# Optimization experiments

Measured on AMD Instinct MI355X. Metric: run time of the kernel, lower is better.

The kernel has to match this reference:

```python
import jax, jax.numpy as jnp
import numpy as np

N_ = 50000   # nodes
E_ = 800000  # edges
G_ = 64      # graphs in batch
EPS = 1e-5   # batchnorm eps


def _lin(k, fi, fo):
    s = 1.0 / np.sqrt(fi)
    return jax.random.uniform(k, (fi, fo), jnp.float32, -s, s)


def setup_inputs() -> dict:
    key = jax.random.key(0)
    ks = jax.random.split(key, 16)
    d_in, d_h, d_out = 128, 128, 5000
    inp = {
        'x': jax.random.normal(ks[0], (N_, d_in), jnp.float32),
        'edge_index': jax.random.randint(ks[1], (2, E_), 0, N_, jnp.int32),
        'batch': jnp.sort(jax.random.randint(ks[2], (N_,), 0, G_, jnp.int32)),
    }
    dims = [(d_in, d_h), (d_h, d_h), (d_h, d_h), (d_h, d_h)]
    for i, (fi, fo) in enumerate(dims, 1):
        inp[f'w{i}'] = _lin(ks[2 + i], fi, fo)
        inp[f'b{i}'] = jnp.zeros((fo,), jnp.float32)
        inp[f'g{i}'] = jnp.ones((fo,), jnp.float32)   # BN gamma
        inp[f'be{i}'] = jnp.zeros((fo,), jnp.float32)  # BN beta
    inp['gw1'] = _lin(ks[7], d_h, d_h // 2)
    inp['gb1'] = jnp.zeros((d_h // 2,), jnp.float32)
    inp['gw2'] = _lin(ks[8], d_h // 2, 1)
    inp['gb2'] = jnp.zeros((1,), jnp.float32)
    inp['cw'] = _lin(ks[9], d_h, d_out)
    inp['cb'] = jnp.zeros((d_out,), jnp.float32)
    return inp


def reference(x, w1, b1, g1, be1, w2, b2, g2, be2, w3, b3, g3, be3,
              w4, b4, g4, be4, gw1, gb1, gw2, gb2, cw, cb,
              edge_index, batch):
    # GCN normalization with self-loops (PyG GCNConv semantics)
    loops = jnp.arange(N_, dtype=edge_index.dtype)
    src = jnp.concatenate([edge_index[0], loops])
    dst = jnp.concatenate([edge_index[1], loops])
    deg = jax.ops.segment_sum(jnp.ones(src.shape[0], jnp.float32), dst, N_)
    dis = jax.lax.rsqrt(jnp.maximum(deg, 1.0))  # deg >= 1 with self-loops
    norm = dis[src] * dis[dst]                  # [E+N]

    def gcn(h, w, b):
        hw = h @ w                              # [N, d]
        msg = hw[src] * norm[:, None]           # gather over edges
        return jax.ops.segment_sum(msg, dst, N_) + b

    def bn(h, g, be):
        m = h.mean(0)
        v = h.var(0)                            # biased var (training BN)
        return (h - m) * jax.lax.rsqrt(v + EPS) * g + be

    h = x
    for w, b, g, be in ((w1, b1, g1, be1), (w2, b2, g2, be2),
                        (w3, b3, g3, be3), (w4, b4, g4, be4)):
        h = jax.nn.relu(bn(gcn(h, w, b), g, be))  # dropout is identity (eval)

    # attention pooling: per-graph softmax over gate scores
    gate = jax.nn.relu(h @ gw1 + gb1) @ gw2 + gb2  # [N, 1]
    gate = gate[:, 0]
    m = jax.ops.segment_max(gate, batch, G_)
    e = jnp.exp(gate - m[batch])
    s = jax.ops.segment_sum(e, batch, G_)
    a = e / s[batch]                               # [N]
    pooled = jax.ops.segment_sum(h * a[:, None], batch, G_)  # [G, d]
    return pooled @ cw + cb                        # [G, out]
```

## Files before the change

kernel.cpp:

```cpp
#include <hip/hip_runtime.h>
#include <hip/hip_bf16.h>
#include <hip/hip_fp16.h>

#define NN   50000
#define NE   800000
#define NG   64
#define DH   128
#define DOUT 5000
#define BNEPS 1e-5f
#define NBLK 196
#define KB   32

__global__ __launch_bounds__(256) void k_count(const int* __restrict__ dst, int* __restrict__ cnt) {
    int e = blockIdx.x * 256 + threadIdx.x;
    if (e < NE) atomicAdd(&cnt[dst[e]], 1);
}

__global__ __launch_bounds__(256) void k_blkscan(const int* __restrict__ cnt, int* __restrict__ rowptr,
                                                 int* __restrict__ bsum) {
    __shared__ int s[256];
    int t = threadIdx.x, i = blockIdx.x * 256 + t;
    int v = (i < NN) ? cnt[i] : 0;
    s[t] = v;
    __syncthreads();
    for (int off = 1; off < 256; off <<= 1) {
        int x = (t >= off) ? s[t - off] : 0;
        __syncthreads();
        s[t] += x;
        __syncthreads();
    }
    if (i < NN) rowptr[i] = s[t] - v;
    if (t == 255) bsum[blockIdx.x] = s[255];
}

__global__ __launch_bounds__(256) void k_bscan(const int* __restrict__ bsum, int* __restrict__ boff) {
    __shared__ int s[256];
    int t = threadIdx.x;
    int v = (t < NBLK) ? bsum[t] : 0;
    s[t] = v;
    __syncthreads();
    for (int off = 1; off < 256; off <<= 1) {
        int x = (t >= off) ? s[t - off] : 0;
        __syncthreads();
        s[t] += x;
        __syncthreads();
    }
    if (t < NBLK) boff[t] = s[t] - v;
}

__global__ __launch_bounds__(256) void k_fin(int* __restrict__ rowptr, const int* __restrict__ boff,
                                             int* __restrict__ cnt, float* __restrict__ dis) {
    int i = blockIdx.x * 256 + threadIdx.x;
    if (i >= NN) { if (i == NN) rowptr[NN] = NE; return; }
    rowptr[i] += boff[blockIdx.x];
    dis[i] = rsqrtf((float)(cnt[i] + 1));
    cnt[i] = 0;
}

__global__ __launch_bounds__(256) void k_fill(const int* __restrict__ ei, const int* __restrict__ rowptr,
                                              int* __restrict__ fil, const float* __restrict__ dis,
                                              int* __restrict__ col, float* __restrict__ wgt) {
    int e = blockIdx.x * 256 + threadIdx.x;
    if (e >= NE) return;
    int s = ei[e], d = ei[NE + e];
    int p = rowptr[d] + atomicAdd(&fil[d], 1);
    col[p] = s;
    wgt[p] = dis[s] * dis[d];
}

__global__ __launch_bounds__(256) void k_gemm2(const float* __restrict__ X, const float* __restrict__ W,
                                               const float* __restrict__ scale, const float* __restrict__ shift,
                                               __half* __restrict__ Y) {
    __shared__ float Xt[KB][DH + 1];
    __shared__ float Ws[KB][DH];
    int t = threadIdx.x;
    int row0 = blockIdx.x * 128;
    int ra = (t >> 4) * 4;
    int ca = (t & 15) * 4;
    float acc[8][8];
#pragma unroll
    for (int i = 0; i < 8; i++)
#pragma unroll
        for (int j = 0; j < 8; j++) acc[i][j] = 0.f;

    for (int kt = 0; kt < DH / KB; kt++) {
        __syncthreads();
#pragma unroll
        for (int i = 0; i < 4; i++) {
            int f = t + i * 256;
            int row = f >> 3;
            int kq = f & 7;
            int grow = min(row0 + row, NN - 1);
            float4 v = ((const float4*)X)[grow * (DH / 4) + kt * 8 + kq];
            if (scale) {
                float4 sc = ((const float4*)scale)[kt * 8 + kq];
                float4 sh = ((const float4*)shift)[kt * 8 + kq];
                v.x = fmaxf(fmaf(v.x, sc.x, sh.x), 0.f);
                v.y = fmaxf(fmaf(v.y, sc.y, sh.y), 0.f);
                v.z = fmaxf(fmaf(v.z, sc.z, sh.z), 0.f);
                v.w = fmaxf(fmaf(v.w, sc.w, sh.w), 0.f);
            }
            Xt[kq * 4 + 0][row] = v.x;
            Xt[kq * 4 + 1][row] = v.y;
            Xt[kq * 4 + 2][row] = v.z;
            Xt[kq * 4 + 3][row] = v.w;
        }
#pragma unroll
        for (int i = 0; i < 4; i++) {
            int f = t + i * 256;
            int k = f >> 5;
            int cq = f & 31;
            float4 wv = ((const float4*)W)[(kt * KB + k) * (DH / 4) + cq];
            *(float4*)&Ws[k][cq * 4] = wv;
        }
        __syncthreads();
#pragma unroll 8
        for (int k = 0; k < KB; k++) {
            float ar[8], bc[8];
            ar[0] = Xt[k][ra + 0];  ar[1] = Xt[k][ra + 1];
            ar[2] = Xt[k][ra + 2];  ar[3] = Xt[k][ra + 3];
            ar[4] = Xt[k][ra + 64]; ar[5] = Xt[k][ra + 65];
            ar[6] = Xt[k][ra + 66]; ar[7] = Xt[k][ra + 67];
            float4 b0 = *(const float4*)&Ws[k][ca];
            float4 b1 = *(const float4*)&Ws[k][ca + 64];
            bc[0] = b0.x; bc[1] = b0.y; bc[2] = b0.z; bc[3] = b0.w;
            bc[4] = b1.x; bc[5] = b1.y; bc[6] = b1.z; bc[7] = b1.w;
#pragma unroll
            for (int ri = 0; ri < 8; ri++)
#pragma unroll
                for (int ci = 0; ci < 8; ci++)
                    acc[ri][ci] = fmaf(ar[ri], bc[ci], acc[ri][ci]);
        }
    }
#pragma unroll
    for (int ri = 0; ri < 8; ri++) {
        int row = row0 + ((ri < 4) ? (ra + ri) : (ra + 60 + ri));
        if (row < NN) {
            __half hv[8];
#pragma unroll
            for (int ci = 0; ci < 8; ci++) hv[ci] = __float2half(acc[ri][ci]);
            *(int2*)(Y + row * DH + ca) = *(int2*)hv;
            *(int2*)(Y + row * DH + ca + 64) = *(int2*)(hv + 4);
        }
    }
}

__global__ __launch_bounds__(256) void k_agg(const __half* __restrict__ HW, const int* __restrict__ rowptr,
                                             const int* __restrict__ col, const float* __restrict__ wgt,
                                             const float* __restrict__ dis, const float* __restrict__ bias,
                                             float* __restrict__ OUT, float* __restrict__ ssum,
                                             float* __restrict__ ssq) {
    __shared__ float lsum[DH], lsq[DH];
    int t = threadIdx.x;
    if (t < DH) { lsum[t] = 0.f; lsq[t] = 0.f; }
    __syncthreads();
    int wid = t >> 6, lane = t & 63;
    int sub = lane >> 5, sl = lane & 31;
    const int2* HW4 = (const int2*)HW;
    float4* OUT4 = (float4*)OUT;
    float4 bv = ((const float4*)bias)[sl];
    float s0 = 0, s1 = 0, s2 = 0, s3 = 0, q0 = 0, q1 = 0, q2 = 0, q3 = 0;
    int gw = blockIdx.x * 4 + wid;
    for (int i = gw * 2 + sub; i < NN; i += 16384) {
        float sd = dis[i];
        int2 hr = HW4[i * 32 + sl];
        float2 f0 = __half22float2(*(__half2*)&hr.x);
        float2 f1 = __half22float2(*(__half2*)&hr.y);
        float a0 = sd * sd * f0.x, a1 = sd * sd * f0.y;
        float a2 = sd * sd * f1.x, a3 = sd * sd * f1.y;
        int p = rowptr[i], p1 = rowptr[i + 1];
        for (; p + 4 <= p1; p += 4) {
            int c0 = col[p], c1 = col[p + 1], c2 = col[p + 2], c3 = col[p + 3];
            float w0 = wgt[p], w1 = wgt[p + 1], w2 = wgt[p + 2], w3 = wgt[p + 3];
            int2 r0 = HW4[c0 * 32 + sl];
            int2 r1 = HW4[c1 * 32 + sl];
            int2 r2 = HW4[c2 * 32 + sl];
            int2 r3 = HW4[c3 * 32 + sl];
            float2 g0 = __half22float2(*(__half2*)&r0.x), g1 = __half22float2(*(__half2*)&r0.y);
            a0 = fmaf(w0, g0.x, a0); a1 = fmaf(w0, g0.y, a1); a2 = fmaf(w0, g1.x, a2); a3 = fmaf(w0, g1.y, a3);
            g0 = __half22float2(*(__half2*)&r1.x); g1 = __half22float2(*(__half2*)&r1.y);
            a0 = fmaf(w1, g0.x, a0); a1 = fmaf(w1, g0.y, a1); a2 = fmaf(w1, g1.x, a2); a3 = fmaf(w1, g1.y, a3);
            g0 = __half22float2(*(__half2*)&r2.x); g1 = __half22float2(*(__half2*)&r2.y);
            a0 = fmaf(w2, g0.x, a0); a1 = fmaf(w2, g0.y, a1); a2 = fmaf(w2, g1.x, a2); a3 = fmaf(w2, g1.y, a3);
            g0 = __half22float2(*(__half2*)&r3.x); g1 = __half22float2(*(__half2*)&r3.y);
            a0 = fmaf(w3, g0.x, a0); a1 = fmaf(w3, g0.y, a1); a2 = fmaf(w3, g1.x, a2); a3 = fmaf(w3, g1.y, a3);
        }
        for (; p < p1; p++) {
            int c = col[p];
            float wv = wgt[p];
            int2 r = HW4[c * 32 + sl];
            float2 g0 = __half22float2(*(__half2*)&r.x), g1 = __half22float2(*(__half2*)&r.y);
            a0 = fmaf(wv, g0.x, a0); a1 = fmaf(wv, g0.y, a1);
            a2 = fmaf(wv, g1.x, a2); a3 = fmaf(wv, g1.y, a3);
        }
        a0 += bv.x; a1 += bv.y; a2 += bv.z; a3 += bv.w;
        OUT4[i * 32 + sl] = make_float4(a0, a1, a2, a3);
        s0 += a0; s1 += a1; s2 += a2; s3 += a3;
        q0 += a0 * a0; q1 += a1 * a1; q2 += a2 * a2; q3 += a3 * a3;
    }
    atomicAdd(&lsum[sl * 4 + 0], s0); atomicAdd(&lsum[sl * 4 + 1], s1);
    atomicAdd(&lsum[sl * 4 + 2], s2); atomicAdd(&lsum[sl * 4 + 3], s3);
    atomicAdd(&lsq[sl * 4 + 0], q0);  atomicAdd(&lsq[sl * 4 + 1], q1);
    atomicAdd(&lsq[sl * 4 + 2], q2);  atomicAdd(&lsq[sl * 4 + 3], q3);
    __syncthreads();
    if (t < DH) { atomicAdd(&ssum[t], lsum[t]); atomicAdd(&ssq[t], lsq[t]); }
}

__global__ void k_bnfin(const float* __restrict__ ssum, const float* __restrict__ ssq,
                        const float* __restrict__ g, const float* __restrict__ be,
                        float* __restrict__ scale, float* __restrict__ shift) {
    int f = threadIdx.x;
    float m = ssum[f] * (1.f / NN);
    float v = ssq[f] * (1.f / NN) - m * m;
    float r = rsqrtf(v + BNEPS);
    float sc = r * g[f];
    scale[f] = sc;
    shift[f] = fmaf(-m, sc, be[f]);
}

__global__ __launch_bounds__(256) void k_bnrelu(float* __restrict__ A, const float* __restrict__ scale,
                                                const float* __restrict__ shift) {
    __shared__ float sc[DH], sh[DH];
    if (threadIdx.x < DH) { sc[threadIdx.x] = scale[threadIdx.x]; sh[threadIdx.x] = shift[threadIdx.x]; }
    __syncthreads();
    float4* A4 = (float4*)A;
    const int total = NN * (DH / 4);
    for (int i = blockIdx.x * 256 + threadIdx.x; i < total; i += gridDim.x * 256) {
        int f = (i & 31) * 4;
        float4 v = A4[i];
        v.x = fmaxf(fmaf(v.x, sc[f], sh[f]), 0.f);
        v.y = fmaxf(fmaf(v.y, sc[f + 1], sh[f + 1]), 0.f);
        v.z = fmaxf(fmaf(v.z, sc[f + 2], sh[f + 2]), 0.f);
        v.w = fmaxf(fmaf(v.w, sc[f + 3], sh[f + 3]), 0.f);
        A4[i] = v;
    }
}

__global__ __launch_bounds__(256) void k_gate(const float* __restrict__ H, const float* __restrict__ gw1,
                                              const float* __restrict__ gb1, const float* __restrict__ gw2,
                                              const float* __restrict__ gb2, float* __restrict__ gate) {
    __shared__ float w1s[DH * 64];
    __shared__ float rowbuf[4][DH];
    int t = threadIdx.x;
    for (int i = t; i < DH * 64; i += 256) w1s[i] = gw1[i];
    __syncthreads();
    int wid = t >> 6, lane = t & 63;
    float b1v = gb1[lane], w2v = gw2[lane], b2v = gb2[0];
    int nw = gridDim.x * 4;
    int iters = (NN + nw - 1) / nw;
    const float2* H2 = (const float2*)H;
    for (int it = 0; it < iters; it++) {
        int i = blockIdx.x * 4 + wid + it * nw;
        bool act = i < NN;
        if (act) {
            float2 hv = H2[i * 64 + lane];
            rowbuf[wid][lane * 2] = hv.x;
            rowbuf[wid][lane * 2 + 1] = hv.y;
        }
        __syncthreads();
        float hid = 0.f;
#pragma unroll 8
        for (int k = 0; k < DH; k++) hid = fmaf(rowbuf[wid][k], w1s[k * 64 + lane], hid);
        hid = fmaxf(hid + b1v, 0.f);
        float v = hid * w2v;
        for (int off = 32; off > 0; off >>= 1) v += __shfl_down(v, off, 64);
        if (act && lane == 0) gate[i] = v + b2v;
        __syncthreads();
    }
}

__device__ __forceinline__ int lbound(const int* __restrict__ a, int v) {
    int lo = 0, hi = NN;
    while (lo < hi) {
        int mid = (lo + hi) >> 1;
        if (a[mid] < v) lo = mid + 1; else hi = mid;
    }
    return lo;
}

__global__ __launch_bounds__(256) void k_pms(const float* __restrict__ gate, const int* __restrict__ batch,
                                             float* __restrict__ ms) {
    __shared__ float red[256];
    int g = blockIdx.x, t = threadIdx.x;
    int s = lbound(batch, g), e = lbound(batch, g + 1);
    float m = -INFINITY;
    for (int i = s + t; i < e; i += 256) m = fmaxf(m, gate[i]);
    red[t] = m; __syncthreads();
    for (int off = 128; off > 0; off >>= 1) { if (t < off) red[t] = fmaxf(red[t], red[t + off]); __syncthreads(); }
    m = red[0];
    __syncthreads();
    float se = 0.f;
    for (int i = s + t; i < e; i += 256) se += __expf(gate[i] - m);
    red[t] = se; __syncthreads();
    for (int off = 128; off > 0; off >>= 1) { if (t < off) red[t] += red[t + off]; __syncthreads(); }
    if (t == 0) {
        ms[g * 2] = m;
        ms[g * 2 + 1] = (e > s) ? 1.f / red[0] : 0.f;
    }
}

#define PNODES 8
__global__ __launch_bounds__(256) void k_pool2(const float* __restrict__ H, const float* __restrict__ gate,
                                               const int* __restrict__ batch, const float* __restrict__ ms,
                                               float* __restrict__ pooled) {
    int wid = threadIdx.x >> 6, lane = threadIdx.x & 63;
    int base = (blockIdx.x * 4 + wid) * PNODES;
    if (base >= NN) return;
    int end = min(base + PNODES, NN);
    const float2* H2 = (const float2*)H;
    float2 acc = make_float2(0.f, 0.f);
    int curg = batch[base];
    for (int i = base; i < end; i++) {
        int g = batch[i];
        if (g != curg) {
            atomicAdd(&pooled[curg * DH + lane * 2], acc.x);
            atomicAdd(&pooled[curg * DH + lane * 2 + 1], acc.y);
            acc = make_float2(0.f, 0.f);
            curg = g;
        }
        float a = __expf(gate[i] - ms[g * 2]) * ms[g * 2 + 1];
        float2 h = H2[i * 64 + lane];
        acc.x = fmaf(a, h.x, acc.x);
        acc.y = fmaf(a, h.y, acc.y);
    }
    atomicAdd(&pooled[curg * DH + lane * 2], acc.x);
    atomicAdd(&pooled[curg * DH + lane * 2 + 1], acc.y);
}

__global__ __launch_bounds__(256) void k_cls(const float* __restrict__ pooled, const float* __restrict__ cw,
                                             const float* __restrict__ cb, float* __restrict__ out) {
    __shared__ float pr[DH];
    int g = blockIdx.y;
    if (threadIdx.x < DH) pr[threadIdx.x] = pooled[g * DH + threadIdx.x];
    __syncthreads();
    int j = blockIdx.x * 256 + threadIdx.x;
    if (j >= DOUT) return;
    float acc = cb[j];
#pragma unroll 8
    for (int k = 0; k < DH; k++) acc = fmaf(pr[k], cw[k * DOUT + j], acc);
    out[g * DOUT + j] = acc;
}

extern "C" void kernel_launch(void* const* d_in, const int* in_sizes, int n_in,
                              void* d_out, int out_size, void* d_ws, size_t ws_size,
                              hipStream_t stream) {
    const float* x     = (const float*)d_in[0];
    const int*   ei    = (const int*)d_in[1];
    const int*   batch = (const int*)d_in[2];
    const float* w[4]  = {(const float*)d_in[3], (const float*)d_in[7], (const float*)d_in[11], (const float*)d_in[15]};
    const float* bb[4] = {(const float*)d_in[4], (const float*)d_in[8], (const float*)d_in[12], (const float*)d_in[16]};
    const float* gg[4] = {(const float*)d_in[5], (const float*)d_in[9], (const float*)d_in[13], (const float*)d_in[17]};
    const float* be[4] = {(const float*)d_in[6], (const float*)d_in[10], (const float*)d_in[14], (const float*)d_in[18]};
    const float* gw1 = (const float*)d_in[19];
    const float* gb1 = (const float*)d_in[20];
    const float* gw2 = (const float*)d_in[21];
    const float* gb2 = (const float*)d_in[22];
    const float* cw  = (const float*)d_in[23];
    const float* cb  = (const float*)d_in[24];

    char* base = (char*)d_ws;
    size_t off = 0;
    auto take = [&](size_t n) -> char* { char* r = base + off; off = (off + n + 255) & ~(size_t)255; return r; };
    float*  bufA   = (float*)take((size_t)NN * DH * 4);
    __half* bufB   = (__half*)take((size_t)NN * DH * 2);
    int*   colv   = (int*)take((size_t)NE * 4);
    float* wgt    = (float*)take((size_t)NE * 4);
    int*   rowptr = (int*)take((size_t)(NN + 1) * 4);
    int*   cnt    = (int*)take((size_t)NN * 4);
    float* dis    = (float*)take((size_t)NN * 4);
    float* gate   = (float*)take((size_t)NN * 4);
    float* stats  = (float*)take(2 * DH * 4);
    float* ssum = stats, *ssq = stats + DH;
    float* scale  = (float*)take(DH * 4);
    float* shift  = (float*)take(DH * 4);
    float* pooled = (float*)take((size_t)NG * DH * 4);
    int*   bsum   = (int*)take((size_t)256 * 4);
    int*   boff   = (int*)take((size_t)256 * 4);
    float* ms     = (float*)take((size_t)NG * 2 * 4);

    hipMemsetAsync(cnt, 0, NN * 4, stream);
    k_count<<<(NE + 255) / 256, 256, 0, stream>>>(ei + NE, cnt);
    k_blkscan<<<NBLK, 256, 0, stream>>>(cnt, rowptr, bsum);
    k_bscan<<<1, 256, 0, stream>>>(bsum, boff);
    k_fin<<<NBLK, 256, 0, stream>>>(rowptr, boff, cnt, dis);
    k_fill<<<(NE + 255) / 256, 256, 0, stream>>>(ei, rowptr, cnt, dis, colv, wgt);

    const int gemm_grid = (NN + 127) / 128;
    for (int L = 0; L < 4; L++) {
        k_gemm2<<<gemm_grid, 256, 0, stream>>>(L == 0 ? x : bufA, w[L],
                                               L == 0 ? nullptr : scale,
                                               L == 0 ? nullptr : shift, bufB);
        hipMemsetAsync(stats, 0, 2 * DH * 4, stream);
        k_agg<<<2048, 256, 0, stream>>>(bufB, rowptr, colv, wgt, dis, bb[L], bufA, ssum, ssq);
        k_bnfin<<<1, DH, 0, stream>>>(ssum, ssq, gg[L], be[L], scale, shift);
    }
    k_bnrelu<<<2048, 256, 0, stream>>>(bufA, scale, shift);
    k_gate<<<1024, 256, 0, stream>>>(bufA, gw1, gb1, gw2, gb2, gate);
    k_pms<<<NG, 256, 0, stream>>>(gate, batch, ms);
    hipMemsetAsync(pooled, 0, (size_t)NG * DH * 4, stream);
    k_pool2<<<(NN + 4 * PNODES - 1) / (4 * PNODES), 256, 0, stream>>>(bufA, gate, batch, ms, pooled);
    k_cls<<<dim3((DOUT + 255) / 256, NG), 256, 0, stream>>>(pooled, cw, cb, (float*)d_out);
}
```

Measured before the change: 658.6 us.

## Use fp16 MFMA for layer GEMMs and fold final BN-ReLU into consumers

Replaces the FP32 register-tiled SIMT GEMM with an MFMA 16x16x32 f16 kernel. The weights are pre-transposed to fp16 once per call, and each lane loads its A and B fragments straight from global memory with no shared-memory staging. The standalone final BN+ReLU pass is removed: the gate and pooling kernels now apply scale and shift on the fly. Stats and pooled zeroing move into bnfin and pms, which drops per-layer memset launches. Converting the inputs to fp16 lowers precision, and fragments fetched uncoalesced from global memory may strain bandwidth.

New measurement: 604.9 us. -8.2%, faster.

```diff
diff --git a/kernel.cpp b/kernel.cpp
--- a/kernel.cpp
+++ b/kernel.cpp
@@ -9,7 +9,9 @@
 #define DOUT 5000
 #define BNEPS 1e-5f
 #define NBLK 196
-#define KB   32
+
+typedef _Float16 h8 __attribute__((ext_vector_type(8)));
+typedef float    f4 __attribute__((ext_vector_type(4)));
 
 __global__ __launch_bounds__(256) void k_count(const int* __restrict__ dst, int* __restrict__ cnt) {
     int e = blockIdx.x * 256 + threadIdx.x;
@@ -68,79 +70,82 @@
     wgt[p] = dis[s] * dis[d];
 }
 
-__global__ __launch_bounds__(256) void k_gemm2(const float* __restrict__ X, const float* __restrict__ W,
+__global__ __launch_bounds__(256) void k_wprep(const float* __restrict__ W0, const float* __restrict__ W1,
+                                               const float* __restrict__ W2, const float* __restrict__ W3,
+                                               __half* __restrict__ Wt) {
+    const float* Ws[4] = {W0, W1, W2, W3};
+    int m = blockIdx.x >> 4;
+    int chunk = blockIdx.x & 15;
+    const float* W = Ws[m];
+    __half* O = Wt + m * DH * DH;
+    int o = chunk * 1024 + threadIdx.x;
+    for (int r = 0; r < 4; r++, o += 256) {
+        int c = o >> 7, k = o & 127;
+        O[o] = __float2half(W[k * DH + c]);
+    }
+}
+
+__global__ __launch_bounds__(256) void k_gemm3(const float* __restrict__ X, const __half* __restrict__ Wt,
                                                const float* __restrict__ scale, const float* __restrict__ shift,
                                                __half* __restrict__ Y) {
-    __shared__ float Xt[KB][DH + 1];
-    __shared__ float Ws[KB][DH];
     int t = threadIdx.x;
-    int row0 = blockIdx.x * 128;
-    int ra = (t >> 4) * 4;
-    int ca = (t & 15) * 4;
-    float acc[8][8];
-#pragma unroll
-    for (int i = 0; i < 8; i++)
-#pragma unroll
-        for (int j = 0; j < 8; j++) acc[i][j] = 0.f;
-
-    for (int kt = 0; kt < DH / KB; kt++) {
-        __syncthreads();
-#pragma unroll
-        for (int i = 0; i < 4; i++) {
-            int f = t + i * 256;
-            int row = f >> 3;
-            int kq = f & 7;
-            int grow = min(row0 + row, NN - 1);
-            float4 v = ((const float4*)X)[grow * (DH / 4) + kt * 8 + kq];
+    int lane = t & 63, wid = t >> 6;
+    int wr = wid >> 1, wc = wid & 1;
+    int row0 = blockIdx.x * 64;
+    int lr = lane & 15, lk = (lane >> 4) * 8;
+
+    f4 acc[2][4];
+#pragma unroll
+    for (int i = 0; i < 2; i++)
+#pragma unroll
+        for (int j = 0; j < 4; j++) acc[i][j] = (f4){0.f, 0.f, 0.f, 0.f};
+
+    for (int kt = 0; kt < 4; kt++) {
+        int kbase = kt * 32 + lk;
+        h8 afr[2];
+#pragma unroll
+        for (int fr = 0; fr < 2; fr++) {
+            int gr = row0 + wr * 32 + fr * 16 + lr;
+            gr = min(gr, NN - 1);
+            const float4* p = (const float4*)(X + (size_t)gr * DH + kbase);
+            float4 v0 = p[0], v1 = p[1];
             if (scale) {
-                float4 sc = ((const float4*)scale)[kt * 8 + kq];
-                float4 sh = ((const float4*)shift)[kt * 8 + kq];
-                v.x = fmaxf(fmaf(v.x, sc.x, sh.x), 0.f);
-                v.y = fmaxf(fmaf(v.y, sc.y, sh.y), 0.f);
-                v.z = fmaxf(fmaf(v.z, sc.z, sh.z), 0.f);
-                v.w = fmaxf(fmaf(v.w, sc.w, sh.w), 0.f);
+                const float4* sc4 = (const float4*)(scale + kbase);
+                const float4* sh4 = (const float4*)(shift + kbase);
+                float4 s0 = sc4[0], s1 = sc4[1], h0 = sh4[0], h1 = sh4[1];
+                v0.x = fmaxf(fmaf(v0.x, s0.x, h0.x), 0.f);
+                v0.y = fmaxf(fmaf(v0.y, s0.y, h0.y), 0.f);
+                v0.z = fmaxf(fmaf(v0.z, s0.z, h0.z), 0.f);
+                v0.w = fmaxf(fmaf(v0.w, s0.w, h0.w), 0.f);
+                v1.x = fmaxf(fmaf(v1.x, s1.x, h1.x), 0.f);
+                v1.y = fmaxf(fmaf(v1.y, s1.y, h1.y), 0.f);
+                v1.z = fmaxf(fmaf(v1.z, s1.z, h1.z), 0.f);
+                v1.w = fmaxf(fmaf(v1.w, s1.w, h1.w), 0.f);
             }
-            Xt[kq * 4 + 0][row] = v.x;
-            Xt[kq * 4 + 1][row] = v.y;
-            Xt[kq * 4 + 2][row] = v.z;
-            Xt[kq * 4 + 3][row] = v.w;
-        }
-#pragma unroll
-        for (int i = 0; i < 4; i++) {
-            int f = t + i * 256;
-            int k = f >> 5;
-            int cq = f & 31;
-            float4 wv = ((const float4*)W)[(kt * KB + k) * (DH / 4) + cq];
-            *(float4*)&Ws[k][cq * 4] = wv;
-        }
-        __syncthreads();
-#pragma unroll 8
-        for (int k = 0; k < KB; k++) {
-            float ar[8], bc[8];
-            ar[0] = Xt[k][ra + 0];  ar[1] = Xt[k][ra + 1];
-            ar[2] = Xt[k][ra + 2];  ar[3] = Xt[k][ra + 3];
-            ar[4] = Xt[k][ra + 64]; ar[5] = Xt[k][ra + 65];
-            ar[6] = Xt[k][ra + 66]; ar[7] = Xt[k][ra + 67];
-            float4 b0 = *(const float4*)&Ws[k][ca];
-            float4 b1 = *(const float4*)&Ws[k][ca + 64];
-            bc[0] = b0.x; bc[1] = b0.y; bc[2] = b0.z; bc[3] = b0.w;
-            bc[4] = b1.x; bc[5] = b1.y; bc[6] = b1.z; bc[7] = b1.w;
-#pragma unroll
-            for (int ri = 0; ri < 8; ri++)
-#pragma unroll
-                for (int ci = 0; ci < 8; ci++)
-                    acc[ri][ci] = fmaf(ar[ri], bc[ci], acc[ri][ci]);
-        }
-    }
-#pragma unroll
-    for (int ri = 0; ri < 8; ri++) {
-        int row = row0 + ((ri < 4) ? (ra + ri) : (ra + 60 + ri));
-        if (row < NN) {
-            __half hv[8];
-#pragma unroll
-            for (int ci = 0; ci < 8; ci++) hv[ci] = __float2half(acc[ri][ci]);
-            *(int2*)(Y + row * DH + ca) = *(int2*)hv;
-            *(int2*)(Y + row * DH + ca + 64) = *(int2*)(hv + 4);
+            h8 a;
+            a[0] = (_Float16)v0.x; a[1] = (_Float16)v0.y; a[2] = (_Float16)v0.z; a[3] = (_Float16)v0.w;
+            a[4] = (_Float16)v1.x; a[5] = (_Float16)v1.y; a[6] = (_Float16)v1.z; a[7] = (_Float16)v1.w;
+            afr[fr] = a;
+        }
+#pragma unroll
+        for (int fc = 0; fc < 4; fc++) {
+            int gc = wc * 64 + fc * 16 + lr;
+            h8 b = *(const h8*)(Wt + (size_t)gc * DH + kbase);
+#pragma unroll
+            for (int fr = 0; fr < 2; fr++)
+                acc[fr][fc] = __builtin_amdgcn_mfma_f32_16x16x32_f16(afr[fr], b, acc[fr][fc], 0, 0, 0);
+        }
+    }
+#pragma unroll
+    for (int fr = 0; fr < 2; fr++) {
+#pragma unroll
+        for (int fc = 0; fc < 4; fc++) {
+            int C = wc * 64 + fc * 16 + lr;
+#pragma unroll
+            for (int q = 0; q < 4; q++) {
+                int R = row0 + wr * 32 + fr * 16 + (lane >> 4) * 4 + q;
+                if (R < NN) Y[(size_t)R * DH + C] = __float2half(acc[fr][fc][q]);
+            }
         }
     }
 }
@@ -206,7 +211,7 @@
     if (t < DH) { atomicAdd(&ssum[t], lsum[t]); atomicAdd(&ssq[t], lsq[t]); }
 }
 
-__global__ void k_bnfin(const float* __restrict__ ssum, const float* __restrict__ ssq,
+__global__ void k_bnfin(float* __restrict__ ssum, float* __restrict__ ssq,
                         const float* __restrict__ g, const float* __restrict__ be,
                         float* __restrict__ scale, float* __restrict__ shift) {
     int f = threadIdx.x;
@@ -216,27 +221,12 @@
     float sc = r * g[f];
     scale[f] = sc;
     shift[f] = fmaf(-m, sc, be[f]);
-}
-
-__global__ __launch_bounds__(256) void k_bnrelu(float* __restrict__ A, const float* __restrict__ scale,
-                                                const float* __restrict__ shift) {
-    __shared__ float sc[DH], sh[DH];
-    if (threadIdx.x < DH) { sc[threadIdx.x] = scale[threadIdx.x]; sh[threadIdx.x] = shift[threadIdx.x]; }
-    __syncthreads();
-    float4* A4 = (float4*)A;
-    const int total = NN * (DH / 4);
-    for (int i = blockIdx.x * 256 + threadIdx.x; i < total; i += gridDim.x * 256) {
-        int f = (i & 31) * 4;
-        float4 v = A4[i];
-        v.x = fmaxf(fmaf(v.x, sc[f], sh[f]), 0.f);
-        v.y = fmaxf(fmaf(v.y, sc[f + 1], sh[f + 1]), 0.f);
-        v.z = fmaxf(fmaf(v.z, sc[f + 2], sh[f + 2]), 0.f);
-        v.w = fmaxf(fmaf(v.w, sc[f + 3], sh[f + 3]), 0.f);
-        A4[i] = v;
-    }
-}
-
-__global__ __launch_bounds__(256) void k_gate(const float* __restrict__ H, const float* __restrict__ gw1,
+    ssum[f] = 0.f;
+    ssq[f] = 0.f;
+}
+
+__global__ __launch_bounds__(256) void k_gate(const float* __restrict__ H, const float* __restrict__ scale,
+                                              const float* __restrict__ shift, const float* __restrict__ gw1,
                                               const float* __restrict__ gb1, const float* __restrict__ gw2,
                                               const float* __restrict__ gb2, float* __restrict__ gate) {
     __shared__ float w1s[DH * 64];
@@ -246,6 +236,8 @@
     __syncthreads();
     int wid = t >> 6, lane = t & 63;
     float b1v = gb1[lane], w2v = gw2[lane], b2v = gb2[0];
+    float2 sc2 = ((const float2*)scale)[lane];
+    float2 sh2 = ((const float2*)shift)[lane];
     int nw = gridDim.x * 4;
     int iters = (NN + nw - 1) / nw;
     const float2* H2 = (const float2*)H;
@@ -254,8 +246,8 @@
         bool act = i < NN;
         if (act) {
             float2 hv = H2[i * 64 + lane];
-            rowbuf[wid][lane * 2] = hv.x;
-            rowbuf[wid][lane * 2 + 1] = hv.y;
+            rowbuf[wid][lane * 2] = fmaxf(fmaf(hv.x, sc2.x, sh2.x), 0.f);
+            rowbuf[wid][lane * 2 + 1] = fmaxf(fmaf(hv.y, sc2.y, sh2.y), 0.f);
         }
         __syncthreads();
         float hid = 0.f;
@@ -279,9 +271,10 @@
 }
 
 __global__ __launch_bounds__(256) void k_pms(const float* __restrict__ gate, const int* __restrict__ batch,
-                                             float* __restrict__ ms) {
+                                             float* __restrict__ ms, float* __restrict__ pooled) {
     __shared__ float red[256];
     int g = blockIdx.x, t = threadIdx.x;
+    if (t < DH) pooled[g * DH + t] = 0.f;
     int s = lbound(batch, g), e = lbound(batch, g + 1);
     float m = -INFINITY;
     for (int i = s + t; i < e; i += 256) m = fmaxf(m, gate[i]);
@@ -300,7 +293,8 @@
 }
 
 #define PNODES 8
-__global__ __launch_bounds__(256) void k_pool2(const float* __restrict__ H, const float* __restrict__ gate,
+__global__ __launch_bounds__(256) void k_pool2(const float* __restrict__ H, const float* __restrict__ scale,
+                                               const float* __restrict__ shift, const float* __restrict__ gate,
                                                const int* __restrict__ batch, const float* __restrict__ ms,
                                                float* __restrict__ pooled) {
     int wid = threadIdx.x >> 6, lane = threadIdx.x & 63;
@@ -308,6 +302,8 @@
     if (base >= NN) return;
     int end = min(base + PNODES, NN);
     const float2* H2 = (const float2*)H;
+    float2 sc2 = ((const float2*)scale)[lane];
+    float2 sh2 = ((const float2*)shift)[lane];
     float2 acc = make_float2(0.f, 0.f);
     int curg = batch[base];
     for (int i = base; i < end; i++) {
@@ -320,8 +316,10 @@
         }
         float a = __expf(gate[i] - ms[g * 2]) * ms[g * 2 + 1];
         float2 h = H2[i * 64 + lane];
-        acc.x = fmaf(a, h.x, acc.x);
-        acc.y = fmaf(a, h.y, acc.y);
+        float hx = fmaxf(fmaf(h.x, sc2.x, sh2.x), 0.f);
+        float hy = fmaxf(fmaf(h.y, sc2.y, sh2.y), 0.f);
+        acc.x = fmaf(a, hx, acc.x);
+        acc.y = fmaf(a, hy, acc.y);
     }
     atomicAdd(&pooled[curg * DH + lane * 2], acc.x);
     atomicAdd(&pooled[curg * DH + lane * 2 + 1], acc.y);
@@ -377,27 +375,27 @@
     int*   bsum   = (int*)take((size_t)256 * 4);
     int*   boff   = (int*)take((size_t)256 * 4);
     float* ms     = (float*)take((size_t)NG * 2 * 4);
+    __half* Wt    = (__half*)take((size_t)4 * DH * DH * 2);
 
     hipMemsetAsync(cnt, 0, NN * 4, stream);
+    hipMemsetAsync(stats, 0, 2 * DH * 4, stream);
     k_count<<<(NE + 255) / 256, 256, 0, stream>>>(ei + NE, cnt);
     k_blkscan<<<NBLK, 256, 0, stream>>>(cnt, rowptr, bsum);
     k_bscan<<<1, 256, 0, stream>>>(bsum, boff);
     k_fin<<<NBLK, 256, 0, stream>>>(rowptr, boff, cnt, dis);
     k_fill<<<(NE + 255) / 256, 256, 0, stream>>>(ei, rowptr, cnt, dis, colv, wgt);
-
-    const int gemm_grid = (NN + 127) / 128;
+    k_wprep<<<64, 256, 0, stream>>>(w[0], w[1], w[2], w[3], Wt);
+
+    const int gemm_grid = (NN + 63) / 64;
     for (int L = 0; L < 4; L++) {
-        k_gemm2<<<gemm_grid, 256, 0, stream>>>(L == 0 ? x : bufA, w[L],
+        k_gemm3<<<gemm_grid, 256, 0, stream>>>(L == 0 ? x : bufA, Wt + (size_t)L * DH * DH,
                                                L == 0 ? nullptr : scale,
                                                L == 0 ? nullptr : shift, bufB);
-        hipMemsetAsync(stats, 0, 2 * DH * 4, stream);
         k_agg<<<2048, 256, 0, stream>>>(bufB, rowptr, colv, wgt, dis, bb[L], bufA, ssum, ssq);
         k_bnfin<<<1, DH, 0, stream>>>(ssum, ssq, gg[L], be[L], scale, shift);
     }
-    k_bnrelu<<<2048, 256, 0, stream>>>(bufA, scale, shift);
-    k_gate<<<1024, 256, 0, stream>>>(bufA, gw1, gb1, gw2, gb2, gate);
-    k_pms<<<NG, 256, 0, stream>>>(gate, batch, ms);
-    hipMemsetAsync(pooled, 0, (size_t)NG * DH * 4, stream);
-    k_pool2<<<(NN + 4 * PNODES - 1) / (4 * PNODES), 256, 0, stream>>>(bufA, gate, batch, ms, pooled);
+    k_gate<<<1024, 256, 0, stream>>>(bufA, scale, shift, gw1, gb1, gw2, gb2, gate);
+    k_pms<<<NG, 256, 0, stream>>>(gate, batch, ms, pooled);
+    k_pool2<<<(NN + 4 * PNODES - 1) / (4 * PNODES), 256, 0, stream>>>(bufA, scale, shift, gate, batch, ms, pooled);
     k_cls<<<dim3((DOUT + 255) / 256, NG), 256, 0, stream>>>(pooled, cw, cb, (float*)d_out);
 }
```
